# Optimization experiments

Hardware: AMD Instinct MI355X
Metric: run time of the kernel (lower is better)

The kernel has to match this reference:

```python
import jax, jax.numpy as jnp
import numpy as np

H = 512      # hidden_size
N = 8        # num_heads (each head has full H dims in this module)
B, T = 4, 1024
LN_EPS = 1e-5


def _layernorm(x, gamma, beta):
    mu = jnp.mean(x, axis=-1, keepdims=True)
    var = jnp.mean(jnp.square(x - mu), axis=-1, keepdims=True)
    return (x - mu) * jax.lax.rsqrt(var + LN_EPS) * gamma + beta


def setup_inputs() -> dict:
    key = jax.random.key(0)
    ks = jax.random.split(key, 8)
    s = 0.02
    return {
        "x":   jax.random.normal(ks[0], (B, T, H), dtype=jnp.float32),
        "Wq":  jax.random.normal(ks[1], (H, N * H), dtype=jnp.float32) * s,
        "Wk":  jax.random.normal(ks[2], (H, N * H), dtype=jnp.float32) * s,
        "Wv":  jax.random.normal(ks[3], (H, N * H), dtype=jnp.float32) * s,
        "Wo":  jax.random.normal(ks[4], (N * H, H), dtype=jnp.float32) * s,
        "g1":  jnp.ones((H,), jnp.float32),
        "beta1": jnp.zeros((H,), jnp.float32),
        "Wf1": jax.random.normal(ks[5], (H, 4 * H), dtype=jnp.float32) * s,
        "bf1": jnp.zeros((4 * H,), jnp.float32),
        "Wf2": jax.random.normal(ks[6], (4 * H, H), dtype=jnp.float32) * s,
        "bf2": jnp.zeros((H,), jnp.float32),
        "g2":  jnp.ones((H,), jnp.float32),
        "beta2": jnp.zeros((H,), jnp.float32),
    }


def reference(x, Wq, Wk, Wv, Wo, g1, beta1, Wf1, bf1, Wf2, bf2, g2, beta2):
    b, t, h = x.shape
    n = Wq.shape[1] // h
    # torch .view(B, N, T, H) on a contiguous (B, T, N*H) tensor is a raw
    # row-major reshape (NOT a transpose) -> identical to jnp.reshape.
    Q = (x @ Wq).reshape(b, n, t, h)
    K = (x @ Wk).reshape(b, n, t, h)
    V = (x @ Wv).reshape(b, n, t, h)
    # 'bath,bahT->batT' with K.transpose(2,3) == standard Q @ K^T per (b,a)
    logits = jnp.einsum('bath,baTh->batT', Q, K)
    attn = jax.nn.softmax(logits / (h ** 0.5), axis=-1)
    # repeated 't' in one operand takes the DIAGONAL of attn (torch semantics,
    # matched by numpy/jax einsum): h[b,a,t,:] = attn[b,a,t,t] * V[b,a,t,:]
    hh = jnp.einsum('batt,bath->bath', attn, V)
    hh = hh.reshape(b, t, n * h) @ Wo
    hh = _layernorm(x + hh, g1, beta1)
    ff = jax.nn.relu(hh @ Wf1 + bf1) @ Wf2 + bf2
    return _layernorm(hh + ff, g2, beta2)
```

## Files before the change

### kernel.cpp

```cpp
#include <hip/hip_runtime.h>
#include <stdint.h>


#define LN_EPS 1e-5f

typedef __attribute__((ext_vector_type(8))) short short8;
typedef __attribute__((ext_vector_type(4))) float f32x4;
typedef __attribute__((ext_vector_type(4))) int int4v;

__device__ __forceinline__ unsigned short f2bf(float f) {
    unsigned int u = __float_as_uint(f);
    u = (u + 0x7fffu + ((u >> 16) & 1u)) >> 16;
    return (unsigned short)u;
}
__device__ __forceinline__ float bf2f(unsigned short h) {
    return __uint_as_float(((unsigned int)h) << 16);
}
__device__ __forceinline__ signed char q8(float v, float s) {
    int q = (int)rintf(v * s);
    q = q > 127 ? 127 : (q < -127 ? -127 : q);
    return (signed char)q;
}

__device__ __forceinline__ void llds16(const void* g, void* l) {
    __builtin_amdgcn_global_load_lds(
        (const __attribute__((address_space(1))) void*)g,
        (__attribute__((address_space(3))) void*)l, 16, 0, 0);
}

__global__ __launch_bounds__(256) void gemm_fold(
    const unsigned short* __restrict__ A,
    const unsigned short* __restrict__ Bt,
    const unsigned short* __restrict__ A2,
    const unsigned short* __restrict__ B2,
    signed char* __restrict__ Cv,
    int N, int K, int lda, int ldb,
    long aBatch, long bBatch, long cBatch) {
    __shared__ unsigned short As[128 * 64];
    __shared__ unsigned short Bs[128 * 64];

    const int bx = blockIdx.x, by = blockIdx.y, bz = blockIdx.z;
    const int tid = threadIdx.x;
    const int wid = tid >> 6;
    const int lane = tid & 63;
    const int lr = lane & 15;
    const int kg = lane >> 4;
    const int wr = wid >> 1;
    const int wc = wid & 1;
    const int row0 = by * 128;
    const int col0 = bx * 128;

    const int zf = bz >> 3, za = bz & 7;
    const unsigned short* Ab = (zf ? A2 : A) + (long)za * aBatch;
    const unsigned short* Bb = (zf ? B2 : Bt) + (long)za * bBatch;
    const long cOff = (long)bz * cBatch;

    const int l8 = lane >> 3;
    const int cs = ((lane & 7) ^ l8) * 8;
    unsigned short* ldsA = &As[wid * 2048];
    unsigned short* ldsB = &Bs[wid * 2048];
    const unsigned short* gA = Ab + (long)(row0 + wid * 32 + l8) * lda + cs;
    const unsigned short* gB = Bb + (long)(col0 + wid * 32 + l8) * ldb + cs;

    const int lr7 = lr & 7;
    const int uS0 = ((0 + kg) ^ lr7) * 8;
    const int uS1 = ((4 + kg) ^ lr7) * 8;

    f32x4 acc[4][4];
#pragma unroll
    for (int m = 0; m < 4; ++m)
#pragma unroll
        for (int n = 0; n < 4; ++n)
#pragma unroll
            for (int j = 0; j < 4; ++j) acc[m][n][j] = 0.f;

    for (int kk = 0; kk < K; kk += 64) {
        __syncthreads();
#pragma unroll
        for (int i = 0; i < 4; ++i) {
            llds16(gA + (long)i * 8 * lda + kk, ldsA + i * 512);
            llds16(gB + (long)i * 8 * ldb + kk, ldsB + i * 512);
        }
        __syncthreads();
        short8 a[4][2], b[4][2];
#pragma unroll
        for (int m = 0; m < 4; ++m) {
            const int ro = (wr * 64 + m * 16 + lr) * 64;
            a[m][0] = *(const short8*)&As[ro + uS0];
            a[m][1] = *(const short8*)&As[ro + uS1];
        }
#pragma unroll
        for (int n = 0; n < 4; ++n) {
            const int ro = (wc * 64 + n * 16 + lr) * 64;
            b[n][0] = *(const short8*)&Bs[ro + uS0];
            b[n][1] = *(const short8*)&Bs[ro + uS1];
        }
#pragma unroll
        for (int s = 0; s < 2; ++s)
#pragma unroll
            for (int m = 0; m < 4; ++m)
#pragma unroll
                for (int n = 0; n < 4; ++n)
                    acc[m][n] = __builtin_amdgcn_mfma_f32_16x16x32_bf16(
                        a[m][s], b[n][s], acc[m][n], 0, 0, 0);
    }

#pragma unroll
    for (int m = 0; m < 4; ++m) {
        const int grow = row0 + wr * 64 + m * 16 + kg * 4;
#pragma unroll
        for (int n = 0; n < 4; ++n) {
            const int gcol = col0 + wc * 64 + n * 16 + lr;
#pragma unroll
            for (int j = 0; j < 4; ++j)
                Cv[cOff + (long)(grow + j) * N + gcol] =
                    q8(acc[m][n][j], 2048.f);
        }
    }
}

template <int IM>
__global__ __launch_bounds__(256) void gemm_i8(
    const signed char* __restrict__ Abase,
    const signed char* __restrict__ Bbase,
    signed char* __restrict__ o8,
    unsigned short* __restrict__ o16,
    const float* __restrict__ bias,
    float* __restrict__ dsum, float* __restrict__ ddiag,
    float invs2048) {
    __shared__ signed char As[128 * 128];
    __shared__ signed char Bs[128 * 128];

    const int bx = blockIdx.x, by = blockIdx.y, bz = blockIdx.z;
    const int tid = threadIdx.x;
    const int wid = tid >> 6;
    const int lane = tid & 63;
    const int lr = lane & 15;
    const int kg = lane >> 4;
    const int wr = wid >> 1;
    const int wc = wid & 1;
    const int row0 = by * 128;
    const int col0 = bx * 128;

    int lda, ldb, N, k0 = 0;
    const signed char* Ab;
    const signed char* Bb;
    if (IM == 0) {
        lda = 512; ldb = 512; N = 4096;
        Ab = Abase;
        Bb = Bbase + (long)bz * (4096 * 512);
    } else if (IM == 1) {
        lda = 4096; ldb = 512; N = 1024;
        const int b = bz >> 3, a = bz & 7;
        Ab = Abase + (long)b * (1024 * 4096) + a * 512;
        Bb = Bbase + (long)b * (1024 * 512);
    } else if (IM == 2) {
        lda = 512; ldb = 512; N = 2048;
        Ab = Abase; Bb = Bbase;
    } else {
        lda = 2048; ldb = 2048; N = 512;
        Ab = Abase; Bb = Bbase;
        k0 = bz * 512;
    }

    const int l8 = lane >> 3;
    const int cs = ((lane & 7) ^ l8) * 16;
    signed char* ldsA = &As[wid * 4096];
    signed char* ldsB = &Bs[wid * 4096];
    const signed char* gA = Ab + (long)(row0 + wid * 32 + l8) * lda + k0 + cs;
    const signed char* gB = Bb + (long)(col0 + wid * 32 + l8) * ldb + k0 + cs;

    const int lr7 = lr & 7;
    const int uS0 = ((0 + kg) ^ lr7) * 16;
    const int uS1 = ((4 + kg) ^ lr7) * 16;

    int4v acc[4][4];
#pragma unroll
    for (int m = 0; m < 4; ++m)
#pragma unroll
        for (int n = 0; n < 4; ++n)
#pragma unroll
            for (int j = 0; j < 4; ++j) acc[m][n][j] = 0;

    for (int kt = 0; kt < 4; ++kt) {
        const int kk = kt * 128;
        __syncthreads();
#pragma unroll
        for (int i = 0; i < 4; ++i) {
            llds16(gA + (long)i * 8 * lda + kk, ldsA + i * 1024);
            llds16(gB + (long)i * 8 * ldb + kk, ldsB + i * 1024);
        }
        __syncthreads();
        int4v av[4][2], bv[4][2];
#pragma unroll
        for (int m = 0; m < 4; ++m) {
            const int ro = (wr * 64 + m * 16 + lr) * 128;
            av[m][0] = *(const int4v*)&As[ro + uS0];
            av[m][1] = *(const int4v*)&As[ro + uS1];
        }
#pragma unroll
        for (int n = 0; n < 4; ++n) {
            const int ro = (wc * 64 + n * 16 + lr) * 128;
            bv[n][0] = *(const int4v*)&Bs[ro + uS0];
            bv[n][1] = *(const int4v*)&Bs[ro + uS1];
        }
#pragma unroll
        for (int s = 0; s < 2; ++s)
#pragma unroll
            for (int m = 0; m < 4; ++m)
#pragma unroll
                for (int n = 0; n < 4; ++n)
                    acc[m][n] = __builtin_amdgcn_mfma_i32_16x16x64_i8(
                        av[m][s], bv[n][s], acc[m][n], 0, 0, 0);
    }

    if (IM == 1) {
        const float dq = 1.52587890625e-5f;
        const int hrow0 = bz * 1024 + row0 + wr * 64;
        const bool diagblk = (bx == by) && (wr == wc);
#pragma unroll
        for (int m = 0; m < 4; ++m) {
            float es[4] = {0.f, 0.f, 0.f, 0.f};
#pragma unroll
            for (int n = 0; n < 4; ++n) {
#pragma unroll
                for (int j = 0; j < 4; ++j) {
                    const float e = __expf((float)acc[m][n][j] * dq);
                    es[j] += e;
                    if (diagblk && n == m && lr == kg * 4 + j)
                        ddiag[hrow0 + m * 16 + kg * 4 + j] = e;
                }
            }
#pragma unroll
            for (int j = 0; j < 4; ++j) {
                float s = es[j];
                s += __shfl_xor(s, 1, 64);
                s += __shfl_xor(s, 2, 64);
                s += __shfl_xor(s, 4, 64);
                s += __shfl_xor(s, 8, 64);
                if (lr == 0) atomicAdd(&dsum[hrow0 + m * 16 + kg * 4 + j], s);
            }
        }
        return;
    }

#pragma unroll
    for (int m = 0; m < 4; ++m) {
        const int grow = row0 + wr * 64 + m * 16 + kg * 4;
#pragma unroll
        for (int n = 0; n < 4; ++n) {
            const int gcol = col0 + wc * 64 + n * 16 + lr;
#pragma unroll
            for (int j = 0; j < 4; ++j) {
                if (IM == 0) {
                    const float v = (float)acc[m][n][j] * 1.52587890625e-5f;
                    if (bz == 0)
                        o8[(long)(grow + j) * 4096 + gcol] = q8(v, invs2048);
                    else
                        o8[(long)16777216 + (long)(grow + j) * 4096 + gcol] =
                            q8(v, 128.f);
                } else if (IM == 2) {
                    const float v = fmaxf(
                        fmaf((float)acc[m][n][j], 3.0517578125e-5f,
                             bias[gcol]), 0.f);
                    o8[(long)(grow + j) * 2048 + gcol] = q8(v, 64.f);
                } else {
                    const float v = (float)acc[m][n][j] * 1.52587890625e-5f;
                    o16[(long)bz * 2097152 + (long)(grow + j) * 512 + gcol] =
                        f2bf(v);
                }
            }
        }
    }
}

__global__ __launch_bounds__(256) void transpose_bf16(
    const float* __restrict__ src, unsigned short* __restrict__ dst,
    int R, int C) {
    __shared__ float tile[32][33];
    const int tx = threadIdx.x & 31;
    const int ty = threadIdx.x >> 5;
    const int r0 = blockIdx.y * 32;
    const int c0 = blockIdx.x * 32;
#pragma unroll
    for (int k = 0; k < 4; ++k)
        tile[ty + k * 8][tx] = src[(long)(r0 + ty + k * 8) * C + c0 + tx];
    __syncthreads();
#pragma unroll
    for (int k = 0; k < 4; ++k)
        dst[(long)(c0 + ty + k * 8) * R + r0 + tx] = f2bf(tile[tx][ty + k * 8]);
}

__global__ __launch_bounds__(256) void transpose_i8(
    const float* __restrict__ src, signed char* __restrict__ dst,
    int R, int C) {
    __shared__ float tile[32][33];
    const int tx = threadIdx.x & 31;
    const int ty = threadIdx.x >> 5;
    const int r0 = blockIdx.y * 32;
    const int c0 = blockIdx.x * 32;
#pragma unroll
    for (int k = 0; k < 4; ++k)
        tile[ty + k * 8][tx] = src[(long)(r0 + ty + k * 8) * C + c0 + tx];
    __syncthreads();
#pragma unroll
    for (int k = 0; k < 4; ++k)
        dst[(long)(c0 + ty + k * 8) * R + r0 + tx] =
            q8(tile[tx][ty + k * 8], 1024.f);
}

__global__ __launch_bounds__(256) void convert3_bf16(
    const float* __restrict__ s0, const float* __restrict__ s1,
    const float* __restrict__ s2, unsigned short* __restrict__ dst) {
    const int idx = blockIdx.x * 256 + threadIdx.x;
    const int y = blockIdx.y;
    const float* src = (y == 0) ? s0 : (y == 1) ? s1 : s2;
    float4 a = ((const float4*)src)[idx * 2];
    float4 b = ((const float4*)src)[idx * 2 + 1];
    uint4 o;
    o.x = (unsigned int)f2bf(a.x) | ((unsigned int)f2bf(a.y) << 16);
    o.y = (unsigned int)f2bf(a.z) | ((unsigned int)f2bf(a.w) << 16);
    o.z = (unsigned int)f2bf(b.x) | ((unsigned int)f2bf(b.y) << 16);
    o.w = (unsigned int)f2bf(b.z) | ((unsigned int)f2bf(b.w) << 16);
    ((uint4*)(dst + (long)y * 2097152))[idx] = o;
}

__global__ __launch_bounds__(256) void quant_x_i8(
    const float* __restrict__ x, signed char* __restrict__ xq, int n4) {
    const int idx = blockIdx.x * 256 + threadIdx.x;
    if (idx >= n4) return;
    float4 v = ((const float4*)x)[idx];
    const int q0 = q8(v.x, 32.f), q1 = q8(v.y, 32.f);
    const int q2 = q8(v.z, 32.f), q3 = q8(v.w, 32.f);
    unsigned int packed = (q0 & 0xff) | ((q1 & 0xff) << 8) |
                          ((q2 & 0xff) << 16) | ((q3 & 0xff) << 24);
    ((unsigned int*)xq)[idx] = packed;
}

__device__ __forceinline__ void ln_reduce(float v0, float v1, int tid,
                                          float* sred, float* sred2,
                                          float& mu, float& rs) {
    float sum = v0 + v1;
    float sq = v0 * v0 + v1 * v1;
#pragma unroll
    for (int off = 32; off > 0; off >>= 1) {
        sum += __shfl_down(sum, off, 64);
        sq += __shfl_down(sq, off, 64);
    }
    const int wave = tid >> 6;
    if ((tid & 63) == 0) { sred[wave] = sum; sred2[wave] = sq; }
    __syncthreads();
    if (tid == 0) {
        float s = 0.f, q = 0.f;
#pragma unroll
        for (int w = 0; w < 4; ++w) { s += sred[w]; q += sred2[w]; }
        const float m = s * (1.f / 512.f);
        const float var = q * (1.f / 512.f) - m * m;
        sred[4] = m;
        sred2[4] = rsqrtf(var + LN_EPS);
    }
    __syncthreads();
    mu = sred[4];
    rs = sred2[4];
}

__global__ __launch_bounds__(256) void ln_combine1(
    const float* __restrict__ x, const signed char* __restrict__ Uq,
    const float* __restrict__ dsum, const float* __restrict__ ddiag,
    const float* __restrict__ g, const float* __restrict__ be,
    float* __restrict__ y1, signed char* __restrict__ y1q) {
    __shared__ float sred[8], sred2[8], df[8];
    const int row = blockIdx.x;
    const int tid = threadIdx.x;
    if (tid < 8) {
        const int b = row >> 10, t = row & 1023;
        const int idx = (b * 8 + tid) * 1024 + t;
        df[tid] = ddiag[idx] / dsum[idx] * (1.f / 128.f);
    }
    __syncthreads();
    const long base = (long)row * 512;
    const long ubase = (long)row * 4096;
    float v0 = x[base + tid];
    float v1 = x[base + tid + 256];
#pragma unroll
    for (int a = 0; a < 8; ++a) {
        const float d = df[a];
        const long ub = ubase + a * 512;
        v0 = fmaf(d, (float)Uq[ub + tid], v0);
        v1 = fmaf(d, (float)Uq[ub + tid + 256], v1);
    }
    float mu, rs;
    ln_reduce(v0, v1, tid, sred, sred2, mu, rs);
    const float o0 = (v0 - mu) * rs * g[tid] + be[tid];
    const float o1 = (v1 - mu) * rs * g[tid + 256] + be[tid + 256];
    y1[base + tid] = o0;
    y1[base + tid + 256] = o1;
    y1q[base + tid] = q8(o0, 32.f);
    y1q[base + tid + 256] = q8(o1, 32.f);
}

__global__ __launch_bounds__(256) void ln_combine2(
    const float* __restrict__ y1, const unsigned short* __restrict__ ffp,
    const float* __restrict__ bias, const float* __restrict__ g,
    const float* __restrict__ be, float* __restrict__ out) {
    __shared__ float sred[8], sred2[8];
    const int row = blockIdx.x;
    const int tid = threadIdx.x;
    const long base = (long)row * 512;
    float v0 = y1[base + tid] + bias[tid];
    float v1 = y1[base + tid + 256] + bias[tid + 256];
#pragma unroll
    for (int z = 0; z < 4; ++z) {
        const long fb = (long)z * 2097152 + base;
        v0 += bf2f(ffp[fb + tid]);
        v1 += bf2f(ffp[fb + tid + 256]);
    }
    float mu, rs;
    ln_reduce(v0, v1, tid, sred, sred2, mu, rs);
    out[base + tid] = (v0 - mu) * rs * g[tid] + be[tid];
    out[base + tid + 256] = (v1 - mu) * rs * g[tid + 256] + be[tid + 256];
}

extern "C" void kernel_launch(void* const* d_in, const int* in_sizes, int n_in,
                              void* d_out, int out_size, void* d_ws, size_t ws_size,
                              hipStream_t stream) {
    const float* x     = (const float*)d_in[0];
    const float* Wq    = (const float*)d_in[1];
    const float* Wk    = (const float*)d_in[2];
    const float* Wv    = (const float*)d_in[3];
    const float* Wo    = (const float*)d_in[4];
    const float* g1    = (const float*)d_in[5];
    const float* beta1 = (const float*)d_in[6];
    const float* Wf1   = (const float*)d_in[7];
    const float* bf1   = (const float*)d_in[8];
    const float* Wf2   = (const float*)d_in[9];
    const float* bf2   = (const float*)d_in[10];
    const float* g2    = (const float*)d_in[11];
    const float* beta2 = (const float*)d_in[12];
    float* out = (float*)d_out;

    char* p = (char*)d_ws;
    unsigned short* Wqb  = (unsigned short*)p; p += (long)512 * 4096 * 2;
    unsigned short* Wkb  = (unsigned short*)p; p += (long)512 * 4096 * 2;
    unsigned short* Wvb  = (unsigned short*)p; p += (long)512 * 4096 * 2;
    unsigned short* WoT  = (unsigned short*)p; p += (long)512 * 4096 * 2;
    signed char*  Wf1Tq  = (signed char*)p;    p += (long)2048 * 512;
    signed char*  Wf2Tq  = (signed char*)p;    p += (long)512 * 2048;
    signed char*  Wallq8 = (signed char*)p;    p += (long)8192 * 512;
    signed char*  PUq8   = (signed char*)p;    p += (long)2 * 4096 * 4096;
    signed char*  xq8    = (signed char*)p;    p += (long)4096 * 512;
    signed char*  y1q8   = (signed char*)p;    p += (long)4096 * 512;
    signed char*  f1q8   = (signed char*)p;    p += (long)4096 * 2048;
    float* dsum  = (float*)p; p += (long)32768 * 4;
    float* ddiag = (float*)p; p += (long)32768 * 4;
    float* y1    = (float*)p; p += (long)4096 * 512 * 4;
    unsigned short* ffp = (unsigned short*)p; p += (long)4 * 4096 * 512 * 2;

    const dim3 blk(256);
    const float invs = 0.04419417382415922f;

    convert3_bf16<<<dim3(1024, 3), blk, 0, stream>>>(Wq, Wk, Wv, Wqb);
    quant_x_i8<<<dim3(2048), blk, 0, stream>>>(x, xq8, 4096 * 512 / 4);
    transpose_bf16<<<dim3(512 / 32, 4096 / 32), blk, 0, stream>>>(Wo, WoT, 4096, 512);
    transpose_i8<<<dim3(2048 / 32, 512 / 32), blk, 0, stream>>>(Wf1, Wf1Tq, 512, 2048);
    transpose_i8<<<dim3(512 / 32, 2048 / 32), blk, 0, stream>>>(Wf2, Wf2Tq, 2048, 512);
    hipMemsetAsync(dsum, 0, 32768 * sizeof(float), stream);

    gemm_fold<<<dim3(4, 4, 16), blk, 0, stream>>>(
        Wkb, Wqb, WoT, Wvb, Wallq8,
        512, 512, 4096, 4096, 512, 512, (long)512 * 512);

    gemm_i8<0><<<dim3(32, 32, 2), blk, 0, stream>>>(
        xq8, Wallq8, PUq8, nullptr, nullptr, nullptr, nullptr, invs * 2048.f);

    gemm_i8<1><<<dim3(8, 8, 32), blk, 0, stream>>>(
        PUq8, xq8, nullptr, nullptr, nullptr, dsum, ddiag, 0.f);

    ln_combine1<<<dim3(4096), blk, 0, stream>>>(
        x, PUq8 + (long)16777216, dsum, ddiag, g1, beta1, y1, y1q8);

    gemm_i8<2><<<dim3(16, 32, 1), blk, 0, stream>>>(
        y1q8, Wf1Tq, f1q8, nullptr, bf1, nullptr, nullptr, 0.f);

    gemm_i8<3><<<dim3(4, 32, 4), blk, 0, stream>>>(
        f1q8, Wf2Tq, nullptr, ffp, nullptr, nullptr, nullptr, 0.f);

    ln_combine2<<<dim3(4096), blk, 0, stream>>>(y1, ffp, bf2, g2, beta2, out);
}
```

Measured before the change: 132.8 us.

## Permute GEMM output columns so epilogues write packed 4-byte stores

GEMM epilogues now pack four per-lane output values (from the four n sub-tiles) into one 32-bit or 64-bit store instead of four scattered byte/short stores. To keep results consistent, column order is permuted inside each 64-wide group: x is quantized in permuted order, Wf2 is transposed with a permuted K index, and the layernorm combine kernels read through the inverse permutation. This aims to cut the number of narrow global store transactions, at the cost of permuted layouts threaded through several kernels that must all stay in agreement.

```diff
diff --git a/kernel.cpp b/kernel.cpp
--- a/kernel.cpp
+++ b/kernel.cpp
@@ -20,6 +20,9 @@
     int q = (int)rintf(v * s);
     q = q > 127 ? 127 : (q < -127 ? -127 : q);
     return (signed char)q;
+}
+__device__ __forceinline__ int pperm(int w) {
+    return (w & ~63) + ((w & 15) << 2) + ((w >> 4) & 3);
 }
 
 __device__ __forceinline__ void llds16(const void* g, void* l) {
@@ -105,16 +108,18 @@
                         a[m][s], b[n][s], acc[m][n], 0, 0, 0);
     }
 
+    const int gbase = col0 + wc * 64 + lr * 4;
 #pragma unroll
     for (int m = 0; m < 4; ++m) {
         const int grow = row0 + wr * 64 + m * 16 + kg * 4;
 #pragma unroll
-        for (int n = 0; n < 4; ++n) {
-            const int gcol = col0 + wc * 64 + n * 16 + lr;
-#pragma unroll
-            for (int j = 0; j < 4; ++j)
-                Cv[cOff + (long)(grow + j) * N + gcol] =
-                    q8(acc[m][n][j], 2048.f);
+        for (int j = 0; j < 4; ++j) {
+            unsigned int o = 0;
+#pragma unroll
+            for (int n = 0; n < 4; ++n)
+                o |= (unsigned int)(unsigned char)q8(acc[m][n][j], 2048.f)
+                     << (8 * n);
+            *(unsigned int*)(Cv + cOff + (long)(grow + j) * N + gbase) = o;
         }
     }
 }
@@ -142,23 +147,23 @@
     const int row0 = by * 128;
     const int col0 = bx * 128;
 
-    int lda, ldb, N, k0 = 0;
+    int lda, ldb, k0 = 0;
     const signed char* Ab;
     const signed char* Bb;
     if (IM == 0) {
-        lda = 512; ldb = 512; N = 4096;
+        lda = 512; ldb = 512;
         Ab = Abase;
         Bb = Bbase + (long)bz * (4096 * 512);
     } else if (IM == 1) {
-        lda = 4096; ldb = 512; N = 1024;
+        lda = 4096; ldb = 512;
         const int b = bz >> 3, a = bz & 7;
         Ab = Abase + (long)b * (1024 * 4096) + a * 512;
         Bb = Bbase + (long)b * (1024 * 512);
     } else if (IM == 2) {
-        lda = 512; ldb = 512; N = 2048;
+        lda = 512; ldb = 512;
         Ab = Abase; Bb = Bbase;
     } else {
-        lda = 2048; ldb = 2048; N = 512;
+        lda = 2048; ldb = 2048;
         Ab = Abase; Bb = Bbase;
         k0 = bz * 512;
     }
@@ -244,31 +249,44 @@
         return;
     }
 
+    const int gbase = col0 + wc * 64 + lr * 4;
 #pragma unroll
     for (int m = 0; m < 4; ++m) {
         const int grow = row0 + wr * 64 + m * 16 + kg * 4;
 #pragma unroll
-        for (int n = 0; n < 4; ++n) {
-            const int gcol = col0 + wc * 64 + n * 16 + lr;
-#pragma unroll
-            for (int j = 0; j < 4; ++j) {
-                if (IM == 0) {
+        for (int j = 0; j < 4; ++j) {
+            if (IM == 0) {
+                unsigned int o = 0;
+                const float s = (bz == 0) ? invs2048 : 128.f;
+#pragma unroll
+                for (int n = 0; n < 4; ++n) {
                     const float v = (float)acc[m][n][j] * 1.52587890625e-5f;
-                    if (bz == 0)
-                        o8[(long)(grow + j) * 4096 + gcol] = q8(v, invs2048);
-                    else
-                        o8[(long)16777216 + (long)(grow + j) * 4096 + gcol] =
-                            q8(v, 128.f);
-                } else if (IM == 2) {
+                    o |= (unsigned int)(unsigned char)q8(v, s) << (8 * n);
+                }
+                const long off = (bz == 0) ? 0 : (long)16777216;
+                *(unsigned int*)(o8 + off + (long)(grow + j) * 4096 + gbase) = o;
+            } else if (IM == 2) {
+                unsigned int o = 0;
+#pragma unroll
+                for (int n = 0; n < 4; ++n) {
+                    const int ocol = col0 + wc * 64 + n * 16 + lr;
                     const float v = fmaxf(
                         fmaf((float)acc[m][n][j], 3.0517578125e-5f,
-                             bias[gcol]), 0.f);
-                    o8[(long)(grow + j) * 2048 + gcol] = q8(v, 64.f);
-                } else {
-                    const float v = (float)acc[m][n][j] * 1.52587890625e-5f;
-                    o16[(long)bz * 2097152 + (long)(grow + j) * 512 + gcol] =
-                        f2bf(v);
+                             bias[ocol]), 0.f);
+                    o |= (unsigned int)(unsigned char)q8(v, 64.f) << (8 * n);
                 }
+                *(unsigned int*)(o8 + (long)(grow + j) * 2048 + gbase) = o;
+            } else {
+                unsigned int lo = 0, hi = 0;
+                const float v0 = (float)acc[m][0][j] * 1.52587890625e-5f;
+                const float v1 = (float)acc[m][1][j] * 1.52587890625e-5f;
+                const float v2 = (float)acc[m][2][j] * 1.52587890625e-5f;
+                const float v3 = (float)acc[m][3][j] * 1.52587890625e-5f;
+                lo = (unsigned int)f2bf(v0) | ((unsigned int)f2bf(v1) << 16);
+                hi = (unsigned int)f2bf(v2) | ((unsigned int)f2bf(v3) << 16);
+                uint2 o; o.x = lo; o.y = hi;
+                *(uint2*)(o16 + (long)bz * 2097152 + (long)(grow + j) * 512 +
+                          gbase) = o;
             }
         }
     }
@@ -291,6 +309,7 @@
         dst[(long)(c0 + ty + k * 8) * R + r0 + tx] = f2bf(tile[tx][ty + k * 8]);
 }
 
+template <bool PERM>
 __global__ __launch_bounds__(256) void transpose_i8(
     const float* __restrict__ src, signed char* __restrict__ dst,
     int R, int C) {
@@ -304,9 +323,11 @@
         tile[ty + k * 8][tx] = src[(long)(r0 + ty + k * 8) * C + c0 + tx];
     __syncthreads();
 #pragma unroll
-    for (int k = 0; k < 4; ++k)
-        dst[(long)(c0 + ty + k * 8) * R + r0 + tx] =
-            q8(tile[tx][ty + k * 8], 1024.f);
+    for (int k = 0; k < 4; ++k) {
+        const int r = r0 + tx;
+        const int rc = PERM ? pperm(r) : r;
+        dst[(long)(c0 + ty + k * 8) * R + rc] = q8(tile[tx][ty + k * 8], 1024.f);
+    }
 }
 
 __global__ __launch_bounds__(256) void convert3_bf16(
@@ -325,16 +346,19 @@
     ((uint4*)(dst + (long)y * 2097152))[idx] = o;
 }
 
-__global__ __launch_bounds__(256) void quant_x_i8(
-    const float* __restrict__ x, signed char* __restrict__ xq, int n4) {
+__global__ __launch_bounds__(256) void quant_x_perm(
+    const float* __restrict__ x, signed char* __restrict__ xq) {
     const int idx = blockIdx.x * 256 + threadIdx.x;
-    if (idx >= n4) return;
-    float4 v = ((const float4*)x)[idx];
-    const int q0 = q8(v.x, 32.f), q1 = q8(v.y, 32.f);
-    const int q2 = q8(v.z, 32.f), q3 = q8(v.w, 32.f);
-    unsigned int packed = (q0 & 0xff) | ((q1 & 0xff) << 8) |
-                          ((q2 & 0xff) << 16) | ((q3 & 0xff) << 24);
-    ((unsigned int*)xq)[idx] = packed;
+    const int t = idx >> 7;
+    const int rem = idx & 127;
+    const int g = rem >> 4, lr = rem & 15;
+    const long rb = (long)t * 512 + g * 64;
+    unsigned int o = 0;
+#pragma unroll
+    for (int n = 0; n < 4; ++n)
+        o |= (unsigned int)(unsigned char)q8(x[rb + n * 16 + lr], 32.f)
+             << (8 * n);
+    *(unsigned int*)(xq + rb + lr * 4) = o;
 }
 
 __device__ __forceinline__ void ln_reduce(float v0, float v1, int tid,
@@ -380,14 +404,16 @@
     __syncthreads();
     const long base = (long)row * 512;
     const long ubase = (long)row * 4096;
+    const int p0 = pperm(tid);
+    const int p1 = pperm(tid + 256);
     float v0 = x[base + tid];
     float v1 = x[base + tid + 256];
 #pragma unroll
     for (int a = 0; a < 8; ++a) {
         const float d = df[a];
         const long ub = ubase + a * 512;
-        v0 = fmaf(d, (float)Uq[ub + tid], v0);
-        v1 = fmaf(d, (float)Uq[ub + tid + 256], v1);
+        v0 = fmaf(d, (float)Uq[ub + p0], v0);
+        v1 = fmaf(d, (float)Uq[ub + p1], v1);
     }
     float mu, rs;
     ln_reduce(v0, v1, tid, sred, sred2, mu, rs);
@@ -407,13 +433,15 @@
     const int row = blockIdx.x;
     const int tid = threadIdx.x;
     const long base = (long)row * 512;
+    const int p0 = pperm(tid);
+    const int p1 = pperm(tid + 256);
     float v0 = y1[base + tid] + bias[tid];
     float v1 = y1[base + tid + 256] + bias[tid + 256];
 #pragma unroll
     for (int z = 0; z < 4; ++z) {
         const long fb = (long)z * 2097152 + base;
-        v0 += bf2f(ffp[fb + tid]);
-        v1 += bf2f(ffp[fb + tid + 256]);
+        v0 += bf2f(ffp[fb + p0]);
+        v1 += bf2f(ffp[fb + p1]);
     }
     float mu, rs;
     ln_reduce(v0, v1, tid, sred, sred2, mu, rs);
@@ -460,10 +488,10 @@
     const float invs = 0.04419417382415922f;
 
     convert3_bf16<<<dim3(1024, 3), blk, 0, stream>>>(Wq, Wk, Wv, Wqb);
-    quant_x_i8<<<dim3(2048), blk, 0, stream>>>(x, xq8, 4096 * 512 / 4);
+    quant_x_perm<<<dim3(2048), blk, 0, stream>>>(x, xq8);
     transpose_bf16<<<dim3(512 / 32, 4096 / 32), blk, 0, stream>>>(Wo, WoT, 4096, 512);
-    transpose_i8<<<dim3(2048 / 32, 512 / 32), blk, 0, stream>>>(Wf1, Wf1Tq, 512, 2048);
-    transpose_i8<<<dim3(512 / 32, 2048 / 32), blk, 0, stream>>>(Wf2, Wf2Tq, 2048, 512);
+    transpose_i8<false><<<dim3(2048 / 32, 512 / 32), blk, 0, stream>>>(Wf1, Wf1Tq, 512, 2048);
+    transpose_i8<true><<<dim3(512 / 32, 2048 / 32), blk, 0, stream>>>(Wf2, Wf2Tq, 2048, 512);
     hipMemsetAsync(dsum, 0, 32768 * sizeof(float), stream);
 
     gemm_fold<<<dim3(4, 4, 16), blk, 0, stream>>>(
```

Measured after the change: 131.1 us. No clear change (-1.3%).
